# Optimization experiments

Measured on AMD Instinct MI355X. Metric: run time of the kernel, lower is better.

The kernel has to match this reference:

```python
import jax, jax.numpy as jnp
import numpy as np
from jax import lax

MAX_DISP = 4  # max_displacement; kernel_size = 1


def setup_inputs() -> dict:
    key = jax.random.key(0)
    k1, k2 = jax.random.split(key)
    B, C, H, W = 8, 96, 160, 320
    in1 = jax.random.normal(k1, (B, C, H, W), dtype=jnp.float32)
    in2 = jax.random.normal(k2, (B, C, H, W), dtype=jnp.float32)
    return {"in1": in1, "in2": in2}


def reference(in1, in2):
    """FlowNet/PWC-Net correlation layer, kernel_size=1, max_displacement=4.

    out[b, w, y, x] = mean_c in1[b, c, y, x] * in2[b, c, y+dy, x+dx]
    with zero padding outside, dy = w // 9 - 4, dx = w % 9 - 4
    (matches the torch unfold window ordering).
    """
    pad = MAX_DISP
    B, C, H, W = in1.shape
    in2p = jnp.pad(in2, ((0, 0), (0, 0), (pad, pad), (pad, pad)))
    outs = []
    # fixed 9x9 displacement grid (81 slices) -- not a data-dim loop
    for dy in range(-pad, pad + 1):
        for dx in range(-pad, pad + 1):
            shifted = lax.dynamic_slice(
                in2p, (0, 0, pad + dy, pad + dx), (B, C, H, W)
            )
            outs.append(jnp.mean(in1 * shifted, axis=1))  # [B, H, W]
    return jnp.stack(outs, axis=1)  # [B, 81, H, W]
```

## Files before the change

kernel.cpp:

```cpp
#include <hip/hip_runtime.h>


#define BB 8
#define CC 96
#define HH 160
#define WW 320
#define TY 8
#define TX 32
#define CK 8
#define NCH (CC / CK)
#define HR (TY + 8)
#define SW 44
#define NT 576
#define HW (HH * WW)
#define NSLOT (CK * HR * (SW / 4))
#define NSTG 3

__global__ __launch_bounds__(NT, 4)
void corr_kernel(const float* __restrict__ in1,
                 const float* __restrict__ in2,
                 float* __restrict__ out) {
    const int x0 = blockIdx.x * TX;
    const int y0 = blockIdx.y * TY;
    const int b  = blockIdx.z;

    const int tid  = threadIdx.x;
    const int dy   = tid >> 6;
    const int lane = tid & 63;
    const int yi   = lane >> 3;
    const int xt   = lane & 7;

    __shared__ __align__(16) float s2[CK][HR][SW];

    int goff[NSTG];
    float4* lsl[NSTG];
    bool ok[NSTG];
#pragma unroll
    for (int t = 0; t < NSTG; ++t) {
        const int i = tid + t * NT;
        ok[t] = false; goff[t] = 0; lsl[t] = (float4*)&s2[0][0][0];
        if (i < NSLOT) {
            const int k = i / (HR * 11), rem = i % (HR * 11);
            const int r = rem / 11, c4 = rem % 11;
            lsl[t] = (float4*)&s2[k][r][4 * c4];
            const int yy = y0 + r - 4;
            const int xs = x0 - 4 + 4 * c4;
            if (c4 < 10 && (unsigned)yy < (unsigned)HH &&
                (unsigned)xs <= (unsigned)(WW - 4)) {
                ok[t] = true;
                goff[t] = (k * HH + yy) * WW + xs;
            }
        }
    }

    {
        const float4 z = make_float4(0.f, 0.f, 0.f, 0.f);
        float4* p = (float4*)&s2[0][0][0];
        for (int i = tid; i < NSLOT; i += NT) p[i] = z;
    }

    float acc[9][4];
#pragma unroll
    for (int i = 0; i < 9; ++i)
#pragma unroll
        for (int j = 0; j < 4; ++j) acc[i][j] = 0.0f;

    const float* in1p = in1 + ((size_t)(b * CC) * HH + y0 + yi) * WW + x0 + 4 * xt;

    for (int ch = 0; ch < NCH; ++ch) {
        const int cb = (b * CC + ch * CK) * HW;
        __syncthreads();
#pragma unroll
        for (int t = 0; t < NSTG; ++t)
            if (ok[t]) *lsl[t] = *(const float4*)(in2 + cb + goff[t]);
        __syncthreads();

#pragma unroll
        for (int k = 0; k < CK; ++k) {
            float a[4];
            *(float4*)a = *(const float4*)(in1p + (size_t)(ch * CK + k) * HW);
            float v[12];
#pragma unroll
            for (int q = 0; q < 3; ++q)
                *(float4*)&v[4 * q] = *(const float4*)&s2[k][yi + dy][4 * xt + 4 * q];
#pragma unroll
            for (int dxi = 0; dxi < 9; ++dxi)
#pragma unroll
                for (int xi = 0; xi < 4; ++xi)
                    acc[dxi][xi] = fmaf(a[xi], v[xi + dxi], acc[dxi][xi]);
        }
    }

    const float scale = 1.0f / (float)CC;
#pragma unroll
    for (int dxi = 0; dxi < 9; ++dxi) {
        float4 o = make_float4(acc[dxi][0] * scale, acc[dxi][1] * scale,
                               acc[dxi][2] * scale, acc[dxi][3] * scale);
        float* dst = out +
            (((size_t)(b * 81 + dy * 9 + dxi) * HH + y0 + yi) * WW + x0 + 4 * xt);
        *(float4*)dst = o;
    }
}

extern "C" void kernel_launch(void* const* d_in, const int* in_sizes, int n_in,
                              void* d_out, int out_size, void* d_ws, size_t ws_size,
                              hipStream_t stream) {
    const float* in1 = (const float*)d_in[0];
    const float* in2 = (const float*)d_in[1];
    float* out = (float*)d_out;
    dim3 grid(WW / TX, HH / TY, BB);
    corr_kernel<<<grid, NT, 0, stream>>>(in1, in2, out);
}
```

Before: 305.2 us.

## Split dy range across three workgroups and remap blocks for XCD locality

Each tile is now handled by three smaller workgroups of 192 threads, each covering three of the nine vertical displacements and staging only a 10-row halo of in2 instead of 16 rows. A 1D grid with an XCD-aware block index remap places the three sibling groups and neighbouring tiles on the same XCD so that the in1 and in2 tiles they share can hit the same L2. This cuts shared memory per block and raises the block count for better occupancy and latency hiding. The cost is that in1 is re-read by three blocks and staged halo rows partly overlap between siblings.

```diff
diff --git a/kernel.cpp b/kernel.cpp
--- a/kernel.cpp
+++ b/kernel.cpp
@@ -7,56 +7,70 @@
 #define WW 320
 #define TY 8
 #define TX 32
+#define GG 3
 #define CK 8
 #define NCH (CC / CK)
-#define HR (TY + 8)
+#define HRG 10
 #define SW 44
-#define NT 576
+#define NT (GG * 64)
 #define HW (HH * WW)
-#define NSLOT (CK * HR * (SW / 4))
-#define NSTG 3
+#define NSLOT (CK * HRG * 11)
+#define NSTG 5
+#define NBX (WW / TX)
+#define NBY (HH / TY)
+#define NWG (BB * NBY * NBX * 3)
+#define NXCD 8
+#define CPX (NWG / NXCD)
 
-__global__ __launch_bounds__(NT, 4)
+__global__ __launch_bounds__(NT, 5)
 void corr_kernel(const float* __restrict__ in1,
                  const float* __restrict__ in2,
                  float* __restrict__ out) {
-    const int x0 = blockIdx.x * TX;
-    const int y0 = blockIdx.y * TY;
-    const int b  = blockIdx.z;
+    const int bid = blockIdx.x;
+    const int nid = (bid % NXCD) * CPX + bid / NXCD;
+    const int g   = nid % 3;
+    int t         = nid / 3;
+    const int bx  = t % NBX;  t /= NBX;
+    const int by  = t % NBY;
+    const int b   = t / NBY;
+
+    const int x0 = bx * TX;
+    const int y0 = by * TY;
 
     const int tid  = threadIdx.x;
-    const int dy   = tid >> 6;
+    const int wv   = tid >> 6;
     const int lane = tid & 63;
     const int yi   = lane >> 3;
     const int xt   = lane & 7;
+    const int dyi  = 3 * g + wv;
 
-    __shared__ __align__(16) float s2[CK][HR][SW];
+    __shared__ __align__(16) float s2[CK][HRG][SW];
 
     int goff[NSTG];
     float4* lsl[NSTG];
     bool ok[NSTG];
 #pragma unroll
-    for (int t = 0; t < NSTG; ++t) {
-        const int i = tid + t * NT;
-        ok[t] = false; goff[t] = 0; lsl[t] = (float4*)&s2[0][0][0];
+    for (int s = 0; s < NSTG; ++s) {
+        const int i = tid + s * NT;
+        ok[s] = false; goff[s] = 0; lsl[s] = (float4*)&s2[0][0][0];
         if (i < NSLOT) {
-            const int k = i / (HR * 11), rem = i % (HR * 11);
+            const int k = i / (HRG * 11), rem = i % (HRG * 11);
             const int r = rem / 11, c4 = rem % 11;
-            lsl[t] = (float4*)&s2[k][r][4 * c4];
-            const int yy = y0 + r - 4;
+            lsl[s] = (float4*)&s2[k][r][4 * c4];
+            const int yy = y0 + 3 * g - 4 + r;
             const int xs = x0 - 4 + 4 * c4;
             if (c4 < 10 && (unsigned)yy < (unsigned)HH &&
                 (unsigned)xs <= (unsigned)(WW - 4)) {
-                ok[t] = true;
-                goff[t] = (k * HH + yy) * WW + xs;
+                ok[s] = true;
+                goff[s] = (k * HH + yy) * WW + xs;
             }
         }
     }
 
     {
         const float4 z = make_float4(0.f, 0.f, 0.f, 0.f);
-        float4* p = (float4*)&s2[0][0][0];
-        for (int i = tid; i < NSLOT; i += NT) p[i] = z;
+        float4* p0 = (float4*)&s2[0][0][0];
+        for (int i = tid; i < NSLOT; i += NT) p0[i] = z;
     }
 
     float acc[9][4];
@@ -71,8 +85,8 @@
         const int cb = (b * CC + ch * CK) * HW;
         __syncthreads();
 #pragma unroll
-        for (int t = 0; t < NSTG; ++t)
-            if (ok[t]) *lsl[t] = *(const float4*)(in2 + cb + goff[t]);
+        for (int s = 0; s < NSTG; ++s)
+            if (ok[s]) *lsl[s] = *(const float4*)(in2 + cb + goff[s]);
         __syncthreads();
 
 #pragma unroll
@@ -82,7 +96,8 @@
             float v[12];
 #pragma unroll
             for (int q = 0; q < 3; ++q)
-                *(float4*)&v[4 * q] = *(const float4*)&s2[k][yi + dy][4 * xt + 4 * q];
+                *(float4*)&v[4 * q] =
+                    *(const float4*)&s2[k][yi + wv][4 * xt + 4 * q];
 #pragma unroll
             for (int dxi = 0; dxi < 9; ++dxi)
 #pragma unroll
@@ -97,7 +112,7 @@
         float4 o = make_float4(acc[dxi][0] * scale, acc[dxi][1] * scale,
                                acc[dxi][2] * scale, acc[dxi][3] * scale);
         float* dst = out +
-            (((size_t)(b * 81 + dy * 9 + dxi) * HH + y0 + yi) * WW + x0 + 4 * xt);
+            (((size_t)(b * 81 + dyi * 9 + dxi) * HH + y0 + yi) * WW + x0 + 4 * xt);
         *(float4*)dst = o;
     }
 }
@@ -108,6 +123,5 @@
     const float* in1 = (const float*)d_in[0];
     const float* in2 = (const float*)d_in[1];
     float* out = (float*)d_out;
-    dim3 grid(WW / TX, HH / TY, BB);
-    corr_kernel<<<grid, NT, 0, stream>>>(in1, in2, out);
+    corr_kernel<<<dim3(NWG), dim3(NT), 0, stream>>>(in1, in2, out);
 }
```

Result: slower. 316.1 us (+3.6%).
